# Performance work log

Measured on AMD Instinct MI355X. Metric: run time of the kernel, lower is better.

## Reference

```python
import jax, jax.numpy as jnp
import numpy as np
from jax import lax

B, L, D, H = 48, 512, 384, 384


def setup_inputs() -> dict:
    key = jax.random.key(0)
    ks = jax.random.split(key, 8)
    def w(k, shape, fan):
        return jax.random.normal(k, shape, jnp.float32) / np.float32(np.sqrt(fan))
    return {
        "v": jax.random.normal(ks[0], (B, L, D), jnp.float32),
        "mask": jnp.ones((B, L), jnp.bool_),
        "Wp_cur": w(ks[1], (D, H), D),      # torch Wp (applied to v_i)
        "Wp_seq": w(ks[2], (D, H), D),      # torch Wp_ (applied to all of v)
        "V": w(ks[3], (H,), H),             # torch V: Linear(H, 1, bias=False)
        "W_ih": w(ks[4], (3 * H, 2 * D), 2 * D),  # GRUCell input weights
        "W_hh": w(ks[5], (3 * H, H), H),           # GRUCell hidden weights
        "b_ih": jnp.zeros((3 * H,), jnp.float32),
        "b_hh": jnp.zeros((3 * H,), jnp.float32),
    }


def _forward(v, mask, Wp_cur, Wp_seq, V, W_ih, W_hh, b_ih, b_hh):
    Bv, Lv, _ = v.shape
    Hh = W_hh.shape[1]
    # Torch recomputes Wp_(v) identically every step; hoist it (same math).
    Wpv = jnp.einsum('bld,dh->blh', v, Wp_seq)            # [B,L,H]
    neg = jnp.where(mask, 0.0, -1e30).astype(v.dtype)     # additive attention mask [B,L]

    def step(h, vi):                                       # vi: [B,D], h: [B,H]
        wpi = vi @ Wp_cur                                  # [B,H]
        x = jnp.tanh(Wpv + wpi[:, None, :])                # [B,L,H]
        s = jnp.einsum('blh,h->bl', x, V) + neg            # scores [B,L]
        a = jax.nn.softmax(s, axis=1)                      # masked softmax
        c = jnp.einsum('bl,bld->bd', a, v)                 # context [B,D]
        r = jnp.concatenate([vi, c], axis=1)               # [B,2D]
        gi = r @ W_ih.T + b_ih
        gh = h @ W_hh.T + b_hh
        ir, iz, inn = jnp.split(gi, 3, axis=1)
        hr, hz, hn = jnp.split(gh, 3, axis=1)
        rg = jax.nn.sigmoid(ir + hr)
        zg = jax.nn.sigmoid(iz + hz)
        ng = jnp.tanh(inn + rg * hn)
        hnew = (1.0 - zg) * ng + zg * h                    # PyTorch GRUCell update
        return hnew, hnew

    h0 = jnp.zeros((Bv, Hh), v.dtype)
    h_last, hs = lax.scan(jax.checkpoint(step), h0, jnp.swapaxes(v, 0, 1))
    hs = jnp.swapaxes(hs, 0, 1)                            # [B,L,H]
    # dropout p=0.0 -> identity; h = hs[:, -1]
    return hs, h_last


def reference(v, mask, Wp_cur, Wp_seq, V, W_ih, W_hh, b_ih, b_hh):
    return _forward(v, mask, Wp_cur, Wp_seq, V, W_ih, W_hh, b_ih, b_hh)
```

## Files before the change

kernel.cpp:

```cpp
#include <hip/hip_runtime.h>


typedef unsigned short u16;
typedef unsigned int u32;
typedef short short8 __attribute__((ext_vector_type(8)));
typedef float f32x4 __attribute__((ext_vector_type(4)));
typedef float f4 __attribute__((ext_vector_type(4)));
typedef _Float16 h2_t __attribute__((ext_vector_type(2)));
typedef _Float16 h8_t __attribute__((ext_vector_type(8)));
typedef u32 u32x4 __attribute__((ext_vector_type(4)));

#define BDIM 48
#define LDIM 512
#define DDIM 384
#define HDIM 384

__device__ __forceinline__ float bf2f(u16 u) { return __uint_as_float(((u32)u) << 16); }
__device__ __forceinline__ u16 f2bf(float f) {
  u32 x = __float_as_uint(f);
  u32 r = (x + 0x7fffu + ((x >> 16) & 1u)) >> 16;
  return (u16)r;
}
__device__ __forceinline__ float sigm(float x) {
  return __builtin_amdgcn_rcpf(1.f + exp2f(-1.4426950408889634f * x));
}
__device__ __forceinline__ float tanh_f(float x) {
  float e = exp2f(2.885390081777927f * x);
  return 1.f - 2.f * __builtin_amdgcn_rcpf(e + 1.f);
}

__device__ __forceinline__ void load16(const void* src, long ld, int isf32,
                                       long row, int kbase, short8& o0, short8& o1)
{
  if (isf32) {
    const float* s = (const float*)src + row * ld + kbase;
    f4 q0 = *(const f4*)(s);
    f4 q1 = *(const f4*)(s + 4);
    f4 q2 = *(const f4*)(s + 8);
    f4 q3 = *(const f4*)(s + 12);
    short8 a, b;
    a[0] = (short)f2bf(q0[0]); a[1] = (short)f2bf(q0[1]);
    a[2] = (short)f2bf(q0[2]); a[3] = (short)f2bf(q0[3]);
    a[4] = (short)f2bf(q1[0]); a[5] = (short)f2bf(q1[1]);
    a[6] = (short)f2bf(q1[2]); a[7] = (short)f2bf(q1[3]);
    b[0] = (short)f2bf(q2[0]); b[1] = (short)f2bf(q2[1]);
    b[2] = (short)f2bf(q2[2]); b[3] = (short)f2bf(q2[3]);
    b[4] = (short)f2bf(q3[0]); b[5] = (short)f2bf(q3[1]);
    b[6] = (short)f2bf(q3[2]); b[7] = (short)f2bf(q3[3]);
    o0 = a; o1 = b;
  } else {
    const u16* s = (const u16*)src + row * ld + kbase;
    o0 = *(const short8*)s;
    o1 = *(const short8*)(s + 8);
  }
}

__global__ __launch_bounds__(256) void gemm_bt(
    const void* __restrict__ A1, const void* __restrict__ A2,
    long lda1, long lda2, int ksplit, int a1f, int a2f,
    const void* __restrict__ Bm, long ldb, int bfm,
    u16* __restrict__ Out, int N, int K,
    long strideA, long strideB, long strideO,
    const float* __restrict__ bias, int epi_exp2, int out_bf16)
{
  __shared__ u16 As[128][40];
  __shared__ u16 Bs[128][40];
  const int tid = threadIdx.x;
  const int lane = tid & 63;
  const int w = tid >> 6;
  const int wm = w >> 1, wn = w & 1;
  const int l15 = lane & 15, quad = lane >> 4;
  const long m0 = (long)blockIdx.x * 128;
  const long n0 = (long)blockIdx.y * 128;
  const int z = blockIdx.z;
  const char* A1p = (const char*)A1 + (long)z * strideA * (a1f ? 4 : 2);
  const char* A2p = (const char*)A2 + (long)z * strideA * (a2f ? 4 : 2);
  const char* Bp  = (const char*)Bm + (long)z * strideB * (bfm ? 4 : 2);
  u16* Op = Out + (long)z * strideO;

  const int r2 = tid & 127;
  const int half = tid >> 7;

  f32x4 acc[4][4];
#pragma unroll
  for (int a = 0; a < 4; a++)
#pragma unroll
    for (int c = 0; c < 4; c++) acc[a][c] = (f32x4){0.f, 0.f, 0.f, 0.f};

  for (int k0 = 0; k0 < K; k0 += 32) {
    const void* srcA; long lda; int kk; int af;
    if (k0 < ksplit) { srcA = A1p; lda = lda1; kk = k0; af = a1f; }
    else             { srcA = A2p; lda = lda2; kk = k0 - ksplit; af = a2f; }
    short8 a0, a1, b0, b1;
    load16(srcA, lda, af, m0 + r2, kk + half * 16, a0, a1);
    load16(Bp, ldb, bfm, n0 + r2, k0 + half * 16, b0, b1);
    __syncthreads();
    *(short8*)&As[r2][half * 16] = a0;
    *(short8*)&As[r2][half * 16 + 8] = a1;
    *(short8*)&Bs[r2][half * 16] = b0;
    *(short8*)&Bs[r2][half * 16 + 8] = b1;
    __syncthreads();
    short8 af_[4], bf_[4];
#pragma unroll
    for (int mt = 0; mt < 4; mt++) af_[mt] = *(const short8*)&As[wm * 64 + mt * 16 + l15][quad * 8];
#pragma unroll
    for (int nt = 0; nt < 4; nt++) bf_[nt] = *(const short8*)&Bs[wn * 64 + nt * 16 + l15][quad * 8];
#pragma unroll
    for (int mt = 0; mt < 4; mt++)
#pragma unroll
      for (int nt = 0; nt < 4; nt++)
        acc[mt][nt] = __builtin_amdgcn_mfma_f32_16x16x32_bf16(af_[mt], bf_[nt], acc[mt][nt], 0, 0, 0);
  }

#pragma unroll
  for (int mt = 0; mt < 4; mt++) {
#pragma unroll
    for (int nt = 0; nt < 4; nt++) {
      const long col = n0 + wn * 64 + nt * 16 + l15;
      float bv = bias ? bias[col] : 0.f;
#pragma unroll
      for (int rg = 0; rg < 4; rg++) {
        long row = m0 + wm * 64 + mt * 16 + quad * 4 + rg;
        float vv = acc[mt][nt][rg] + bv;
        if (epi_exp2) {
          float t = vv * 2.885390081777927f;
          t = fminf(fmaxf(t, -15.9f), 15.9f);
          vv = exp2f(t);
        }
        long idx = row * (long)N + col;
        if (out_bf16) Op[idx] = f2bf(vv);
        else ((_Float16*)Op)[idx] = (_Float16)vv;
      }
    }
  }
}

__global__ void transpose_f2b(const float* __restrict__ src, u16* __restrict__ dst,
                              int rows, int cols, long sstride, long dstride)
{
  __shared__ float t[32][33];
  const int bz = blockIdx.z;
  const float* s = src + (long)bz * sstride;
  u16* d = dst + (long)bz * dstride;
  const int c0 = blockIdx.x * 32, r0 = blockIdx.y * 32;
  const int tx = threadIdx.x, ty = threadIdx.y;
#pragma unroll
  for (int j = 0; j < 4; j++) t[ty + j * 8][tx] = s[(long)(r0 + ty + j * 8) * cols + c0 + tx];
  __syncthreads();
#pragma unroll
  for (int j = 0; j < 4; j++) d[(long)(c0 + ty + j * 8) * rows + r0 + tx] = f2bf(t[tx][ty + j * 8]);
}

__global__ __launch_bounds__(256) void attn_softmax(
    const _Float16* __restrict__ E, const _Float16* __restrict__ F,
    const float* __restrict__ Vw, u16* __restrict__ Aout)
{
  const int blk = blockIdx.x;
  const int x8 = blk & 7;
  const int rest = blk >> 3;
  const int i = rest & 511;
  const int b = x8 + 8 * (rest >> 9);
  const int tid = threadIdx.x;
  const int lane = tid & 63, w = tid >> 6;
  const int r = lane & 15, sub = lane >> 4;
  __shared__ float Tl[512];
  __shared__ float red[8];

  const h8_t* Fr = (const h8_t*)(F + ((long)b * LDIM + i) * HDIM + r * 24);
  h8_t fq0 = Fr[0], fq1 = Fr[1], fq2 = Fr[2];
  float fv[24], vv[24];
#pragma unroll
  for (int j = 0; j < 8; j++) {
    fv[j] = (float)fq0[j]; fv[8 + j] = (float)fq1[j]; fv[16 + j] = (float)fq2[j];
  }
  const float* Vp = Vw + r * 24;
#pragma unroll
  for (int j = 0; j < 24; j++) vv[j] = Vp[j];

  for (int li = 0; li < 32; ++li) {
    const int l = li * 16 + w * 4 + sub;
    const h8_t* Er = (const h8_t*)(E + ((long)b * LDIM + l) * HDIM + r * 24);
    h8_t e0 = Er[0], e1 = Er[1], e2 = Er[2];
    float p = 0.f;
#pragma unroll
    for (int j = 0; j < 8; j++) {
      p += vv[j]      * __builtin_amdgcn_rcpf((float)e0[j] * fv[j]      + 1.f);
      p += vv[8 + j]  * __builtin_amdgcn_rcpf((float)e1[j] * fv[8 + j]  + 1.f);
      p += vv[16 + j] * __builtin_amdgcn_rcpf((float)e2[j] * fv[16 + j] + 1.f);
    }
    p += __shfl_xor(p, 1);
    p += __shfl_xor(p, 2);
    p += __shfl_xor(p, 4);
    p += __shfl_xor(p, 8);
    if (r == 0) Tl[l] = p;
  }
  __syncthreads();

  const float t0 = Tl[tid], t1 = Tl[tid + 256];
  float mn = fminf(t0, t1);
#pragma unroll
  for (int off = 32; off; off >>= 1) mn = fminf(mn, __shfl_xor(mn, off));
  if (lane == 0) red[w] = mn;
  __syncthreads();
  const float mT = fminf(fminf(red[0], red[1]), fminf(red[2], red[3]));
  const float C2 = 2.885390081777927f;
  float p0 = exp2f(C2 * (mT - t0));
  float p1 = exp2f(C2 * (mT - t1));
  float ssum = p0 + p1;
#pragma unroll
  for (int off = 32; off; off >>= 1) ssum += __shfl_xor(ssum, off);
  if (lane == 0) red[4 + w] = ssum;
  __syncthreads();
  const float Z = (red[4] + red[5]) + (red[6] + red[7]);
  const float inv = __builtin_amdgcn_rcpf(Z);
  u16* Ar = Aout + ((long)b * LDIM + i) * LDIM;
  Ar[tid] = f2bf(p0 * inv);
  Ar[tid + 256] = f2bf(p1 * inv);
}

__global__ __launch_bounds__(512, 2) void recurrence(
    const float* __restrict__ Whh, const float* __restrict__ bhh_g,
    const _Float16* __restrict__ GI, u32* __restrict__ hslots,
    float* __restrict__ out)
{
  const int blk = blockIdx.x;
  const int x8 = blk & 7;
  const int s = blk >> 3;
  const int b = x8 + 8 * (s % 6);
  const int g = s / 6;
  const int tid = threadIdx.x;
  const int tx = tid & 15;
  const int ty = tid >> 4;
  const int jbase = g * 96 + ty * 3;

  __shared__ __align__(16) u16 hall[2][HDIM];

  h2_t wv[9][12];
  float bh[9];
#pragma unroll
  for (int q = 0; q < 9; q++) {
    const int R = (q % 3) * 384 + jbase + (q / 3);
    const f4* wq = (const f4*)(Whh + (long)R * HDIM + tx * 24);
#pragma unroll
    for (int t6 = 0; t6 < 6; t6++) {
      f4 u = wq[t6];
      wv[q][2 * t6]     = (h2_t){(_Float16)u[0], (_Float16)u[1]};
      wv[q][2 * t6 + 1] = (h2_t){(_Float16)u[2], (_Float16)u[3]};
    }
    bh[q] = bhh_g[R];
  }

  float gc[9], gn[9];
#pragma unroll
  for (int q = 0; q < 9; q++) gn[q] = 0.f;
  if (tx == 0) {
    const _Float16* gp = GI + (long)b * LDIM * 1152 + jbase;
#pragma unroll
    for (int q = 0; q < 9; q++) gn[q] = (float)gp[(q % 3) * 384 + (q / 3)];
  }

  const int SLOT = BDIM * HDIM;
  const u32* pollp = hslots + (long)b * HDIM + tid;
  u32* sf = hslots + (long)b * HDIM + jbase;
  const int remote = (tid < HDIM) && ((tid / 96) != g);

  float hp0 = 0.f, hp1 = 0.f, hp2 = 0.f;
  u16 hu0 = 0, hu1 = 0, hu2 = 0;

  for (int i = 0; i < LDIM; ++i) {
#pragma unroll
    for (int q = 0; q < 9; q++) gc[q] = gn[q];

    if (tx == 0 && i + 1 < LDIM) {
      const _Float16* gp = GI + ((long)b * LDIM + (i + 1)) * 1152 + jbase;
#pragma unroll
      for (int q = 0; q < 9; q++) gn[q] = (float)gp[(q % 3) * 384 + (q / 3)];
    }

    const int buf = i & 1;
    if (i > 0) {
      if (remote) {
        const u32* p = pollp + (buf ? SLOT : 0);
        u32 val = __hip_atomic_load(p, __ATOMIC_RELAXED, __HIP_MEMORY_SCOPE_AGENT);
        while ((val >> 16) != (u32)i) {
          __builtin_amdgcn_s_sleep(1);
          val = __hip_atomic_load(p, __ATOMIC_RELAXED, __HIP_MEMORY_SCOPE_AGENT);
        }
        hall[buf][tid] = (u16)(val & 0xffffu);
      }
      if (tx == 0) {
        hall[buf][jbase]     = hu0;
        hall[buf][jbase + 1] = hu1;
        hall[buf][jbase + 2] = hu2;
      }
      __syncthreads();
    }

    float ac[9];
    if (i > 0) {
      union { u32x4 q4[3]; h2_t h[12]; } hv;
      const u32x4* h4 = (const u32x4*)&hall[buf][tx * 24];
      hv.q4[0] = h4[0]; hv.q4[1] = h4[1]; hv.q4[2] = h4[2];
#pragma unroll
      for (int q = 0; q < 9; q++) {
        float a = 0.f;
#pragma unroll
        for (int p = 0; p < 12; p++) a = __builtin_amdgcn_fdot2(wv[q][p], hv.h[p], a, false);
        a += __shfl_xor(a, 1);
        a += __shfl_xor(a, 2);
        a += __shfl_xor(a, 4);
        a += __shfl_xor(a, 8);
        ac[q] = a;
      }
    } else {
#pragma unroll
      for (int q = 0; q < 9; q++) ac[q] = 0.f;
    }

    if (tx == 0) {
      float h0n, h1n, h2n;
      {
        float rg = sigm(gc[0] + ac[0] + bh[0]);
        float zg = sigm(gc[1] + ac[1] + bh[1]);
        float ng = tanh_f(gc[2] + rg * (ac[2] + bh[2]));
        h0n = (1.f - zg) * ng + zg * hp0;
      }
      {
        float rg = sigm(gc[3] + ac[3] + bh[3]);
        float zg = sigm(gc[4] + ac[4] + bh[4]);
        float ng = tanh_f(gc[5] + rg * (ac[5] + bh[5]));
        h1n = (1.f - zg) * ng + zg * hp1;
      }
      {
        float rg = sigm(gc[6] + ac[6] + bh[6]);
        float zg = sigm(gc[7] + ac[7] + bh[7]);
        float ng = tanh_f(gc[8] + rg * (ac[8] + bh[8]));
        h2n = (1.f - zg) * ng + zg * hp2;
      }
      union { _Float16 h; u16 u; } c0, c1, c2;
      c0.h = (_Float16)h0n; c1.h = (_Float16)h1n; c2.h = (_Float16)h2n;
      if (i + 1 < LDIM) {
        u32* sp = sf + (((i + 1) & 1) ? SLOT : 0);
        const u32 t = (u32)(i + 1) << 16;
        __hip_atomic_store(sp + 0, t | (u32)c0.u, __ATOMIC_RELAXED, __HIP_MEMORY_SCOPE_AGENT);
        __hip_atomic_store(sp + 1, t | (u32)c1.u, __ATOMIC_RELAXED, __HIP_MEMORY_SCOPE_AGENT);
        __hip_atomic_store(sp + 2, t | (u32)c2.u, __ATOMIC_RELAXED, __HIP_MEMORY_SCOPE_AGENT);
      }
      hp0 = h0n; hp1 = h1n; hp2 = h2n;
      hu0 = c0.u; hu1 = c1.u; hu2 = c2.u;
      const long orow = ((long)b * LDIM + i) * HDIM + jbase;
      out[orow] = h0n; out[orow + 1] = h1n; out[orow + 2] = h2n;
      if (i == LDIM - 1) {
        const long fo = (long)BDIM * LDIM * HDIM + (long)b * HDIM + jbase;
        out[fo] = h0n; out[fo + 1] = h1n; out[fo + 2] = h2n;
      }
    }
  }
}

extern "C" void kernel_launch(void* const* d_in, const int* in_sizes, int n_in,
                              void* d_out, int out_size, void* d_ws, size_t ws_size,
                              hipStream_t stream)
{
  (void)in_sizes; (void)n_in; (void)out_size; (void)ws_size;
  const float* v      = (const float*)d_in[0];
  const float* Wp_cur = (const float*)d_in[2];
  const float* Wp_seq = (const float*)d_in[3];
  const float* Vw     = (const float*)d_in[4];
  const float* W_ih   = (const float*)d_in[5];
  const float* W_hh   = (const float*)d_in[6];
  const float* b_ih   = (const float*)d_in[7];
  const float* b_hh   = (const float*)d_in[8];
  float* out = (float*)d_out;

  char* ws = (char*)d_ws;
  size_t off = 0;
  auto alloc = [&](size_t bytes) -> char* {
    char* p = ws + off;
    off += (bytes + 255) & ~(size_t)255;
    return p;
  };
  u32* hslots = (u32*)alloc((size_t)2 * 48 * 384 * 4);
  u16* WpSeqT = (u16*)alloc((size_t)384 * 384 * 2);
  u16* WpCurT = (u16*)alloc((size_t)384 * 384 * 2);
  u16* Cbuf   = (u16*)alloc((size_t)24576 * 384 * 2);
  u16* vT     = (u16*)alloc((size_t)48 * 384 * 512 * 2);
  char* region = alloc((size_t)24576 * 384 * 2 * 2 + (size_t)24576 * 512 * 2);
  _Float16* E  = (_Float16*)region;
  _Float16* F  = (_Float16*)(region + (size_t)24576 * 384 * 2);
  u16* Abuf    = (u16*)(region + (size_t)24576 * 384 * 2 * 2);
  _Float16* GI = (_Float16*)region;

  transpose_f2b<<<dim3(12, 12, 1), dim3(32, 8), 0, stream>>>(Wp_seq, WpSeqT, 384, 384, 0, 0);
  transpose_f2b<<<dim3(12, 12, 1), dim3(32, 8), 0, stream>>>(Wp_cur, WpCurT, 384, 384, 0, 0);
  transpose_f2b<<<dim3(12, 16, 48), dim3(32, 8), 0, stream>>>(v, vT, 512, 384,
                                                              (long)512 * 384, (long)384 * 512);

  gemm_bt<<<dim3(192, 3, 1), 256, 0, stream>>>(v, v, 384, 384, 1 << 30, 1, 1,
                                               WpSeqT, 384, 0,
                                               (u16*)E, 384, 384, 0, 0, 0, nullptr, 1, 0);
  gemm_bt<<<dim3(192, 3, 1), 256, 0, stream>>>(v, v, 384, 384, 1 << 30, 1, 1,
                                               WpCurT, 384, 0,
                                               (u16*)F, 384, 384, 0, 0, 0, nullptr, 1, 0);

  attn_softmax<<<dim3(24576), 256, 0, stream>>>(E, F, Vw, Abuf);

  gemm_bt<<<dim3(4, 3, 48), 256, 0, stream>>>(Abuf, Abuf, 512, 512, 1 << 30, 0, 0,
                                              vT, 512, 0,
                                              Cbuf, 384, 512,
                                              (long)512 * 512, (long)384 * 512, (long)512 * 384,
                                              nullptr, 0, 1);

  gemm_bt<<<dim3(192, 9, 1), 256, 0, stream>>>(v, Cbuf, 384, 384, 384, 1, 0,
                                               W_ih, 768, 1,
                                               (u16*)GI, 1152, 768, 0, 0, 0, b_ih, 0, 0);

  void* args[] = {(void*)&W_hh, (void*)&b_hh, (void*)&GI, (void*)&hslots, (void*)&out};
  hipLaunchCooperativeKernel(recurrence, dim3(192), dim3(512), args, 0, stream);
}
```

Before: 2.346 ms.

## Pin GRU recurrence groups to one XCC and poll h through XCC-local cache

Each recurrence block reads its hardware XCC id and claims a role from a per-XCC counter, so that all four column groups of a batch row run on the same XCC. The h exchange then uses sc0 loads and stores, which can be served from the XCC-local L2 instead of device-scope memory, with a mirrored agent-scope copy as a fallback after a spin limit. The grid is enlarged to 256 blocks to cover XCC imbalance, and surplus blocks exit after a grid sync. This adds two grid syncs, duplicate stores, a memset and a reliance on undocumented coherence behaviour, and the GI prefetch is moved after the wait.

```diff
diff --git a/kernel.cpp b/kernel.cpp
--- a/kernel.cpp
+++ b/kernel.cpp
@@ -1,5 +1,8 @@
 #include <hip/hip_runtime.h>
-
+#include <hip/hip_cooperative_groups.h>
+
+
+namespace cg = cooperative_groups;
 
 typedef unsigned short u16;
 typedef unsigned int u32;
@@ -27,6 +30,16 @@
 __device__ __forceinline__ float tanh_f(float x) {
   float e = exp2f(2.885390081777927f * x);
   return 1.f - 2.f * __builtin_amdgcn_rcpf(e + 1.f);
+}
+
+__device__ __forceinline__ u32 ld_sc0(const u32* p) {
+  u32 v;
+  asm volatile("global_load_dword %0, %1, off sc0\n\ts_waitcnt vmcnt(0)"
+               : "=v"(v) : "v"(p) : "memory");
+  return v;
+}
+__device__ __forceinline__ void st_sc0(u32* p, u32 v) {
+  asm volatile("global_store_dword %0, %1, off sc0" :: "v"(p), "v"(v) : "memory");
 }
 
 __device__ __forceinline__ void load16(const void* src, long ld, int isf32,
@@ -220,48 +233,79 @@
 
 __global__ __launch_bounds__(512, 2) void recurrence(
     const float* __restrict__ Whh, const float* __restrict__ bhh_g,
-    const _Float16* __restrict__ GI, u32* __restrict__ hslots,
-    float* __restrict__ out)
-{
-  const int blk = blockIdx.x;
-  const int x8 = blk & 7;
-  const int s = blk >> 3;
-  const int b = x8 + 8 * (s % 6);
-  const int g = s / 6;
+    const _Float16* __restrict__ GI, u32* __restrict__ claim,
+    u32* __restrict__ hfast, u32* __restrict__ hmir, float* __restrict__ out)
+{
   const int tid = threadIdx.x;
   const int tx = tid & 15;
   const int ty = tid >> 4;
+
+  __shared__ int srole;
+  __shared__ int sfall;
+  __shared__ __align__(16) u16 hall[2][HDIM];
+
+  int xcc;
+  asm volatile("s_getreg_b32 %0, hwreg(HW_REG_XCC_ID)" : "=s"(xcc));
+  xcc &= 7;
+  if (tid == 0) {
+    sfall = 0;
+    u32 t = __hip_atomic_fetch_add(&claim[xcc], 1u, __ATOMIC_RELAXED, __HIP_MEMORY_SCOPE_AGENT);
+    if (t < 24u) srole = xcc * 24 + (int)t;
+    else srole = -1 - (int)__hip_atomic_fetch_add(&claim[8], 1u, __ATOMIC_RELAXED,
+                                                  __HIP_MEMORY_SCOPE_AGENT);
+  }
+  cg::this_grid().sync();
+  if (tid == 0 && srole < 0) {
+    int rank = -1 - srole, acc = 0, r = -1;
+    for (int x = 0; x < 8; x++) {
+      int c = (int)__hip_atomic_load(&claim[x], __ATOMIC_RELAXED, __HIP_MEMORY_SCOPE_AGENT);
+      int have = c < 24 ? c : 24;
+      int d = 24 - have;
+      if (r < 0 && rank < acc + d) r = x * 24 + have + (rank - acc);
+      acc += d;
+    }
+    srole = r;
+  }
+  __syncthreads();
+  const int role = srole;
+  const bool active = (role >= 0);
+  const int b = active ? (role / 24) * 6 + (role % 24) / 4 : 0;
+  const int g = active ? (role & 3) : 0;
   const int jbase = g * 96 + ty * 3;
-
-  __shared__ __align__(16) u16 hall[2][HDIM];
 
   h2_t wv[9][12];
   float bh[9];
-#pragma unroll
-  for (int q = 0; q < 9; q++) {
-    const int R = (q % 3) * 384 + jbase + (q / 3);
-    const f4* wq = (const f4*)(Whh + (long)R * HDIM + tx * 24);
-#pragma unroll
-    for (int t6 = 0; t6 < 6; t6++) {
-      f4 u = wq[t6];
-      wv[q][2 * t6]     = (h2_t){(_Float16)u[0], (_Float16)u[1]};
-      wv[q][2 * t6 + 1] = (h2_t){(_Float16)u[2], (_Float16)u[3]};
-    }
-    bh[q] = bhh_g[R];
-  }
-
   float gc[9], gn[9];
 #pragma unroll
   for (int q = 0; q < 9; q++) gn[q] = 0.f;
-  if (tx == 0) {
-    const _Float16* gp = GI + (long)b * LDIM * 1152 + jbase;
-#pragma unroll
-    for (int q = 0; q < 9; q++) gn[q] = (float)gp[(q % 3) * 384 + (q / 3)];
-  }
+  if (active) {
+#pragma unroll
+    for (int q = 0; q < 9; q++) {
+      const int R = (q % 3) * 384 + jbase + (q / 3);
+      const f4* wq = (const f4*)(Whh + (long)R * HDIM + tx * 24);
+#pragma unroll
+      for (int t6 = 0; t6 < 6; t6++) {
+        f4 u = wq[t6];
+        wv[q][2 * t6]     = (h2_t){(_Float16)u[0], (_Float16)u[1]};
+        wv[q][2 * t6 + 1] = (h2_t){(_Float16)u[2], (_Float16)u[3]};
+      }
+      bh[q] = bhh_g[R];
+    }
+    if (tx == 0) {
+      const _Float16* gp = GI + (long)b * LDIM * 1152 + jbase;
+#pragma unroll
+      for (int q = 0; q < 9; q++) gn[q] = (float)gp[(q % 3) * 384 + (q / 3)];
+    }
+  }
+  cg::this_grid().sync();
+  if (!active) return;
 
   const int SLOT = BDIM * HDIM;
-  const u32* pollp = hslots + (long)b * HDIM + tid;
-  u32* sf = hslots + (long)b * HDIM + jbase;
+  const long poff = (long)b * HDIM + tid;
+  const u32* pfF = hfast + poff;
+  const u32* pfM = hmir + poff;
+  u32* sfF = hfast + (long)b * HDIM + jbase;
+  u32* sfM = hmir + (long)b * HDIM + jbase;
   const int remote = (tid < HDIM) && ((tid / 96) != g);
 
   float hp0 = 0.f, hp1 = 0.f, hp2 = 0.f;
@@ -270,21 +314,28 @@
   for (int i = 0; i < LDIM; ++i) {
 #pragma unroll
     for (int q = 0; q < 9; q++) gc[q] = gn[q];
-
-    if (tx == 0 && i + 1 < LDIM) {
-      const _Float16* gp = GI + ((long)b * LDIM + (i + 1)) * 1152 + jbase;
-#pragma unroll
-      for (int q = 0; q < 9; q++) gn[q] = (float)gp[(q % 3) * 384 + (q / 3)];
-    }
 
     const int buf = i & 1;
     if (i > 0) {
       if (remote) {
-        const u32* p = pollp + (buf ? SLOT : 0);
-        u32 val = __hip_atomic_load(p, __ATOMIC_RELAXED, __HIP_MEMORY_SCOPE_AGENT);
-        while ((val >> 16) != (u32)i) {
-          __builtin_amdgcn_s_sleep(1);
-          val = __hip_atomic_load(p, __ATOMIC_RELAXED, __HIP_MEMORY_SCOPE_AGENT);
+        const int o = buf ? SLOT : 0;
+        const int fbf = sfall;
+        u32 val = 0;
+        if (!fbf) {
+          val = ld_sc0(pfF + o);
+          int spins = 0;
+          while ((val >> 16) != (u32)i) {
+            if (++spins > 512) { sfall = 1; break; }
+            __builtin_amdgcn_s_sleep(1);
+            val = ld_sc0(pfF + o);
+          }
+        }
+        if ((val >> 16) != (u32)i) {
+          val = __hip_atomic_load(pfM + o, __ATOMIC_RELAXED, __HIP_MEMORY_SCOPE_AGENT);
+          while ((val >> 16) != (u32)i) {
+            __builtin_amdgcn_s_sleep(1);
+            val = __hip_atomic_load(pfM + o, __ATOMIC_RELAXED, __HIP_MEMORY_SCOPE_AGENT);
+          }
         }
         hall[buf][tid] = (u16)(val & 0xffffu);
       }
@@ -294,6 +345,12 @@
         hall[buf][jbase + 2] = hu2;
       }
       __syncthreads();
+    }
+
+    if (tx == 0 && i + 1 < LDIM) {
+      const _Float16* gp = GI + ((long)b * LDIM + (i + 1)) * 1152 + jbase;
+#pragma unroll
+      for (int q = 0; q < 9; q++) gn[q] = (float)gp[(q % 3) * 384 + (q / 3)];
     }
 
     float ac[9];
@@ -340,11 +397,15 @@
       union { _Float16 h; u16 u; } c0, c1, c2;
       c0.h = (_Float16)h0n; c1.h = (_Float16)h1n; c2.h = (_Float16)h2n;
       if (i + 1 < LDIM) {
-        u32* sp = sf + (((i + 1) & 1) ? SLOT : 0);
+        const int o = (((i + 1) & 1) ? SLOT : 0);
         const u32 t = (u32)(i + 1) << 16;
-        __hip_atomic_store(sp + 0, t | (u32)c0.u, __ATOMIC_RELAXED, __HIP_MEMORY_SCOPE_AGENT);
-        __hip_atomic_store(sp + 1, t | (u32)c1.u, __ATOMIC_RELAXED, __HIP_MEMORY_SCOPE_AGENT);
-        __hip_atomic_store(sp + 2, t | (u32)c2.u, __ATOMIC_RELAXED, __HIP_MEMORY_SCOPE_AGENT);
+        const u32 v0 = t | (u32)c0.u, v1 = t | (u32)c1.u, v2 = t | (u32)c2.u;
+        st_sc0(sfF + o + 0, v0);
+        st_sc0(sfF + o + 1, v1);
+        st_sc0(sfF + o + 2, v2);
+        __hip_atomic_store(sfM + o + 0, v0, __ATOMIC_RELAXED, __HIP_MEMORY_SCOPE_AGENT);
+        __hip_atomic_store(sfM + o + 1, v1, __ATOMIC_RELAXED, __HIP_MEMORY_SCOPE_AGENT);
+        __hip_atomic_store(sfM + o + 2, v2, __ATOMIC_RELAXED, __HIP_MEMORY_SCOPE_AGENT);
       }
       hp0 = h0n; hp1 = h1n; hp2 = h2n;
       hu0 = c0.u; hu1 = c1.u; hu2 = c2.u;
@@ -380,7 +441,9 @@
     off += (bytes + 255) & ~(size_t)255;
     return p;
   };
-  u32* hslots = (u32*)alloc((size_t)2 * 48 * 384 * 4);
+  u32* claim  = (u32*)alloc(64);
+  u32* hfast  = (u32*)alloc((size_t)2 * 48 * 384 * 4);
+  u32* hmir   = (u32*)alloc((size_t)2 * 48 * 384 * 4);
   u16* WpSeqT = (u16*)alloc((size_t)384 * 384 * 2);
   u16* WpCurT = (u16*)alloc((size_t)384 * 384 * 2);
   u16* Cbuf   = (u16*)alloc((size_t)24576 * 384 * 2);
@@ -391,6 +454,8 @@
   u16* Abuf    = (u16*)(region + (size_t)24576 * 384 * 2 * 2);
   _Float16* GI = (_Float16*)region;
 
+  hipMemsetAsync(claim, 0, 64, stream);
+
   transpose_f2b<<<dim3(12, 12, 1), dim3(32, 8), 0, stream>>>(Wp_seq, WpSeqT, 384, 384, 0, 0);
   transpose_f2b<<<dim3(12, 12, 1), dim3(32, 8), 0, stream>>>(Wp_cur, WpCurT, 384, 384, 0, 0);
   transpose_f2b<<<dim3(12, 16, 48), dim3(32, 8), 0, stream>>>(v, vT, 512, 384,
@@ -415,6 +480,7 @@
                                                W_ih, 768, 1,
                                                (u16*)GI, 1152, 768, 0, 0, 0, b_ih, 0, 0);
 
-  void* args[] = {(void*)&W_hh, (void*)&b_hh, (void*)&GI, (void*)&hslots, (void*)&out};
-  hipLaunchCooperativeKernel(recurrence, dim3(192), dim3(512), args, 0, stream);
-}
+  void* args[] = {(void*)&W_hh, (void*)&b_hh, (void*)&GI, (void*)&claim,
+                  (void*)&hfast, (void*)&hmir, (void*)&out};
+  hipLaunchCooperativeKernel(recurrence, dim3(256), dim3(512), args, 0, stream);
+}
```

New measurement: 2.730 ms. +16.4%, slower.

## Process four query rows per attention block and use DPP row reductions

Applied to the files above, without the earlier changes.

The attention-score kernel now handles four query positions i per block, so each loaded E row is reused across four F rows. This cuts E reloads and the fp16-to-float conversions by a factor of four and reduces the grid to a quarter of the blocks. The softmax is restructured so that each wavefront owns one row and reduces it entirely with shuffles, which removes the shared-memory reduction steps and the extra barriers. The 16-lane sum reductions in both the attention and recurrence kernels are replaced by DPP row_shr adds instead of __shfl_xor, which adds register pressure (four fv arrays) in exchange.

```diff
diff --git a/kernel.cpp b/kernel.cpp
--- a/kernel.cpp
+++ b/kernel.cpp
@@ -27,6 +27,14 @@
 __device__ __forceinline__ float tanh_f(float x) {
   float e = exp2f(2.885390081777927f * x);
   return 1.f - 2.f * __builtin_amdgcn_rcpf(e + 1.f);
+}
+
+__device__ __forceinline__ float red16(float v) {
+  v += __int_as_float(__builtin_amdgcn_update_dpp(0, __float_as_int(v), 0x101, 0xf, 0xf, true));
+  v += __int_as_float(__builtin_amdgcn_update_dpp(0, __float_as_int(v), 0x102, 0xf, 0xf, true));
+  v += __int_as_float(__builtin_amdgcn_update_dpp(0, __float_as_int(v), 0x104, 0xf, 0xf, true));
+  v += __int_as_float(__builtin_amdgcn_update_dpp(0, __float_as_int(v), 0x108, 0xf, 0xf, true));
+  return v;
 }
 
 __device__ __forceinline__ void load16(const void* src, long ld, int isf32,
@@ -158,20 +166,23 @@
   const int blk = blockIdx.x;
   const int x8 = blk & 7;
   const int rest = blk >> 3;
-  const int i = rest & 511;
-  const int b = x8 + 8 * (rest >> 9);
+  const int it = rest & 127;
+  const int b = x8 + 8 * (rest >> 7);
+  const int i0 = it * 4;
   const int tid = threadIdx.x;
   const int lane = tid & 63, w = tid >> 6;
   const int r = lane & 15, sub = lane >> 4;
-  __shared__ float Tl[512];
-  __shared__ float red[8];
-
-  const h8_t* Fr = (const h8_t*)(F + ((long)b * LDIM + i) * HDIM + r * 24);
-  h8_t fq0 = Fr[0], fq1 = Fr[1], fq2 = Fr[2];
-  float fv[24], vv[24];
-#pragma unroll
-  for (int j = 0; j < 8; j++) {
-    fv[j] = (float)fq0[j]; fv[8 + j] = (float)fq1[j]; fv[16 + j] = (float)fq2[j];
+  __shared__ float Tl[4][512];
+
+  float fv[4][24], vv[24];
+#pragma unroll
+  for (int ii = 0; ii < 4; ii++) {
+    const h8_t* Fr = (const h8_t*)(F + ((long)b * LDIM + i0 + ii) * HDIM + r * 24);
+    h8_t f0 = Fr[0], f1 = Fr[1], f2 = Fr[2];
+#pragma unroll
+    for (int j = 0; j < 8; j++) {
+      fv[ii][j] = (float)f0[j]; fv[ii][8 + j] = (float)f1[j]; fv[ii][16 + j] = (float)f2[j];
+    }
   }
   const float* Vp = Vw + r * 24;
 #pragma unroll
@@ -181,41 +192,47 @@
     const int l = li * 16 + w * 4 + sub;
     const h8_t* Er = (const h8_t*)(E + ((long)b * LDIM + l) * HDIM + r * 24);
     h8_t e0 = Er[0], e1 = Er[1], e2 = Er[2];
-    float p = 0.f;
+    float ev[24];
 #pragma unroll
     for (int j = 0; j < 8; j++) {
-      p += vv[j]      * __builtin_amdgcn_rcpf((float)e0[j] * fv[j]      + 1.f);
-      p += vv[8 + j]  * __builtin_amdgcn_rcpf((float)e1[j] * fv[8 + j]  + 1.f);
-      p += vv[16 + j] * __builtin_amdgcn_rcpf((float)e2[j] * fv[16 + j] + 1.f);
-    }
-    p += __shfl_xor(p, 1);
-    p += __shfl_xor(p, 2);
-    p += __shfl_xor(p, 4);
-    p += __shfl_xor(p, 8);
-    if (r == 0) Tl[l] = p;
+      ev[j] = (float)e0[j]; ev[8 + j] = (float)e1[j]; ev[16 + j] = (float)e2[j];
+    }
+    float p0 = 0.f, p1 = 0.f, p2 = 0.f, p3 = 0.f;
+#pragma unroll
+    for (int j = 0; j < 24; j++) {
+      const float e = ev[j], vj = vv[j];
+      p0 += vj * __builtin_amdgcn_rcpf(e * fv[0][j] + 1.f);
+      p1 += vj * __builtin_amdgcn_rcpf(e * fv[1][j] + 1.f);
+      p2 += vj * __builtin_amdgcn_rcpf(e * fv[2][j] + 1.f);
+      p3 += vj * __builtin_amdgcn_rcpf(e * fv[3][j] + 1.f);
+    }
+    p0 = red16(p0); p1 = red16(p1); p2 = red16(p2); p3 = red16(p3);
+    if (r == 0) {
+      Tl[0][l] = p0; Tl[1][l] = p1; Tl[2][l] = p2; Tl[3][l] = p3;
+    }
   }
   __syncthreads();
 
-  const float t0 = Tl[tid], t1 = Tl[tid + 256];
-  float mn = fminf(t0, t1);
-#pragma unroll
-  for (int off = 32; off; off >>= 1) mn = fminf(mn, __shfl_xor(mn, off));
-  if (lane == 0) red[w] = mn;
-  __syncthreads();
-  const float mT = fminf(fminf(red[0], red[1]), fminf(red[2], red[3]));
-  const float C2 = 2.885390081777927f;
-  float p0 = exp2f(C2 * (mT - t0));
-  float p1 = exp2f(C2 * (mT - t1));
-  float ssum = p0 + p1;
-#pragma unroll
-  for (int off = 32; off; off >>= 1) ssum += __shfl_xor(ssum, off);
-  if (lane == 0) red[4 + w] = ssum;
-  __syncthreads();
-  const float Z = (red[4] + red[5]) + (red[6] + red[7]);
-  const float inv = __builtin_amdgcn_rcpf(Z);
-  u16* Ar = Aout + ((long)b * LDIM + i) * LDIM;
-  Ar[tid] = f2bf(p0 * inv);
-  Ar[tid + 256] = f2bf(p1 * inv);
+  {
+    float t[8];
+#pragma unroll
+    for (int k = 0; k < 8; k++) t[k] = Tl[w][lane + k * 64];
+    float mn = t[0];
+#pragma unroll
+    for (int k = 1; k < 8; k++) mn = fminf(mn, t[k]);
+#pragma unroll
+    for (int off = 32; off; off >>= 1) mn = fminf(mn, __shfl_xor(mn, off));
+    const float C2 = 2.885390081777927f;
+    float ps[8], ss = 0.f;
+#pragma unroll
+    for (int k = 0; k < 8; k++) { ps[k] = exp2f(C2 * (mn - t[k])); ss += ps[k]; }
+#pragma unroll
+    for (int off = 32; off; off >>= 1) ss += __shfl_xor(ss, off);
+    const float inv = __builtin_amdgcn_rcpf(ss);
+    u16* Ar = Aout + ((long)b * LDIM + i0 + w) * LDIM;
+#pragma unroll
+    for (int k = 0; k < 8; k++) Ar[lane + k * 64] = f2bf(ps[k] * inv);
+  }
 }
 
 __global__ __launch_bounds__(512, 2) void recurrence(
@@ -306,11 +323,7 @@
         float a = 0.f;
 #pragma unroll
         for (int p = 0; p < 12; p++) a = __builtin_amdgcn_fdot2(wv[q][p], hv.h[p], a, false);
-        a += __shfl_xor(a, 1);
-        a += __shfl_xor(a, 2);
-        a += __shfl_xor(a, 4);
-        a += __shfl_xor(a, 8);
-        ac[q] = a;
+        ac[q] = red16(a);
       }
     } else {
 #pragma unroll
@@ -403,7 +416,7 @@
                                                WpCurT, 384, 0,
                                                (u16*)F, 384, 384, 0, 0, 0, nullptr, 1, 0);
 
-  attn_softmax<<<dim3(24576), 256, 0, stream>>>(E, F, Vw, Abuf);
+  attn_softmax<<<dim3(6144), 256, 0, stream>>>(E, F, Vw, Abuf);
 
   gemm_bt<<<dim3(4, 3, 48), 256, 0, stream>>>(Abuf, Abuf, 512, 512, 1 << 30, 0, 0,
                                               vT, 512, 0,
```

Result: faster. 2.140 ms (-8.8%).
